# Performance work log

Hardware: AMD Instinct MI355X
Metric: run time of the kernel (lower is better)

## Reference

```python
import jax, jax.numpy as jnp
import numpy as np

B, S, D, E, F, K = 2, 1024, 2048, 8, 1024, 2


def setup_inputs() -> dict:
    key = jax.random.key(0)
    ks = jax.random.split(key, 5)
    s = 0.02  # init scale for weights
    return {
        "hidden_states": jax.random.normal(ks[0], (B, S, D), dtype=jnp.float32),
        "gate_w": jax.random.normal(ks[1], (E, D), dtype=jnp.float32) * s,
        "w_gate": jax.random.normal(ks[2], (E, D, F), dtype=jnp.float32) * s,
        "w_up": jax.random.normal(ks[3], (E, D, F), dtype=jnp.float32) * s,
        "w_down": jax.random.normal(ks[4], (E, F, D), dtype=jnp.float32) * s,
        "top_k": K,
    }


def reference(hidden_states, gate_w, w_gate, w_up, w_down, top_k):
    b, s, d = hidden_states.shape
    x = hidden_states.reshape(-1, d)                      # [T, D] tokens
    T = x.shape[0]
    n_exp = gate_w.shape[0]

    # router gate (bias-free linear) + topk softmax
    router_logits = jnp.einsum('td,ed->te', x, gate_w)    # [T, E]
    probs = jax.nn.softmax(router_logits, axis=-1)
    top_w, top_i = jax.lax.top_k(probs, top_k)            # [T, K]
    top_w = top_w / jnp.sum(top_w, axis=-1, keepdims=True)  # renormalize over selected experts

    # scatter routing weights into dense combine matrix [T, E] (zero for unselected experts)
    comb = jnp.zeros((T, n_exp), dtype=x.dtype)
    comb = comb.at[jnp.arange(T)[:, None], top_i].set(top_w)

    # SwiGLU expert MLPs, computed for all experts and masked by routing weights
    g = jax.nn.silu(jnp.einsum('td,edf->etf', x, w_gate))  # [E, T, F]
    u = jnp.einsum('td,edf->etf', x, w_up)                 # [E, T, F]
    h = (g * u) * comb.T[:, :, None]                       # weight before down-proj to fuse combine
    y = jnp.einsum('etf,efd->td', h, w_down)               # [T, D] combined output

    final = y.reshape(b, s, d)
    return final, router_logits
```

## Files before the change

kernel.cpp:

```cpp
#include <hip/hip_runtime.h>
#include <hip/hip_bf16.h>

#define T_TOK 2048
#define D_DIM 2048
#define N_EXP 8
#define F_DIM 1024

typedef __attribute__((ext_vector_type(8))) short short8;
typedef __attribute__((ext_vector_type(4))) float floatx4;

__device__ __forceinline__ short f2bf(float f) {
  union { float f; unsigned u; } v; v.f = f;
  unsigned r = v.u + 0x7fffu + ((v.u >> 16) & 1u);
  return (short)(r >> 16);
}

__device__ __forceinline__ floatx4 mfma16(short8 a, short8 b, floatx4 c) {
  return __builtin_amdgcn_mfma_f32_16x16x32_bf16(a, b, c, 0, 0, 0);
}

__device__ __forceinline__ void gload16(const void* g, void* l) {
  __builtin_amdgcn_global_load_lds(
      (const __attribute__((address_space(1))) unsigned int*)g,
      (__attribute__((address_space(3))) unsigned int*)l, 16, 0, 0);
}

__global__ __launch_bounds__(256) void transpose_cvt(const float* __restrict__ src,
                                                     short* __restrict__ dst,
                                                     int R, int C) {
  __shared__ float tile[32][33];
  int e = blockIdx.z;
  src += (size_t)e * R * C;
  dst += (size_t)e * R * C;
  int c0 = blockIdx.x * 32, r0 = blockIdx.y * 32;
  int tx = threadIdx.x & 31, ty = threadIdx.x >> 5;
#pragma unroll
  for (int i = 0; i < 32; i += 8)
    tile[ty + i][tx] = src[(size_t)(r0 + ty + i) * C + c0 + tx];
  __syncthreads();
#pragma unroll
  for (int i = 0; i < 32; i += 8)
    dst[(size_t)(c0 + ty + i) * R + r0 + tx] = f2bf(tile[tx][ty + i]);
}

__global__ __launch_bounds__(256) void router_kernel(
    const float* __restrict__ x, const float* __restrict__ gate_w,
    short* __restrict__ x_bf, float* __restrict__ out_logits,
    int* __restrict__ counts, int* __restrict__ tok_ids, float* __restrict__ tok_wts) {
  int t = blockIdx.x;
  int tid = threadIdx.x;
  const float* xr = x + (size_t)t * D_DIM + tid * 8;
  floatx4 xv0 = *(const floatx4*)xr;
  floatx4 xv1 = *(const floatx4*)(xr + 4);
  float xs[8];
#pragma unroll
  for (int j = 0; j < 4; j++) { xs[j] = xv0[j]; xs[4 + j] = xv1[j]; }
  union { short8 v; short s[8]; } xb;
#pragma unroll
  for (int j = 0; j < 8; j++) xb.s[j] = f2bf(xs[j]);
  *(short8*)(x_bf + (size_t)t * D_DIM + tid * 8) = xb.v;

  float p[N_EXP];
#pragma unroll
  for (int e = 0; e < N_EXP; e++) {
    const float* gw = gate_w + (size_t)e * D_DIM + tid * 8;
    floatx4 g0 = *(const floatx4*)gw;
    floatx4 g1 = *(const floatx4*)(gw + 4);
    float s = 0.f;
#pragma unroll
    for (int j = 0; j < 4; j++) s += xs[j] * g0[j] + xs[4 + j] * g1[j];
    p[e] = s;
  }
  __shared__ float red[N_EXP * 4];
  __shared__ float slog[N_EXP];
  int lane = tid & 63, wv = tid >> 6;
#pragma unroll
  for (int e = 0; e < N_EXP; e++) {
    float v = p[e];
#pragma unroll
    for (int off = 32; off > 0; off >>= 1) v += __shfl_down(v, off);
    if (lane == 0) red[e * 4 + wv] = v;
  }
  __syncthreads();
  if (tid < N_EXP) {
    float s = red[tid * 4] + red[tid * 4 + 1] + red[tid * 4 + 2] + red[tid * 4 + 3];
    slog[tid] = s;
    out_logits[(size_t)t * N_EXP + tid] = s;
  }
  __syncthreads();
  if (tid == 0) {
    float l[N_EXP];
#pragma unroll
    for (int e = 0; e < N_EXP; e++) l[e] = slog[e];
    int e0 = 0;
#pragma unroll
    for (int e = 1; e < N_EXP; e++) if (l[e] > l[e0]) e0 = e;
    int e1 = (e0 == 0) ? 1 : 0;
#pragma unroll
    for (int e = 0; e < N_EXP; e++) if (e != e0 && l[e] > l[e1]) e1 = e;
    float p1 = __expf(l[e1] - l[e0]);
    float s = 1.f + p1;
    int pos0 = atomicAdd(&counts[e0], 1);
    tok_ids[e0 * T_TOK + pos0] = t;
    tok_wts[e0 * T_TOK + pos0] = 1.f / s;
    int pos1 = atomicAdd(&counts[e1], 1);
    tok_ids[e1 * T_TOK + pos1] = t | (1 << 16);
    tok_wts[e1 * T_TOK + pos1] = p1 / s;
  }
}

__global__ __launch_bounds__(256, 2) void gemm1_kernel(
    const short* __restrict__ x_bf,
    const short* __restrict__ wgT, const short* __restrict__ wuT,
    const int* __restrict__ counts, const int* __restrict__ tok_ids,
    const float* __restrict__ tok_wts,
    short* __restrict__ hbuf) {
  int e = blockIdx.x >> 4;
  int mt = blockIdx.x & 15;
  int count = counts[e];
  if (mt * 128 >= count) return;
  int f0 = blockIdx.y * 128;

  __shared__ short sA[128 * 64];
  __shared__ short sBg[128 * 64];
  __shared__ short sBu[128 * 64];
  __shared__ int s_tok[128];
  __shared__ float s_wt[128];

  int tid = threadIdx.x;
  if (tid < 128) {
    int r = mt * 128 + tid;
    if (r < count) { s_tok[tid] = tok_ids[e * T_TOK + r]; s_wt[tid] = tok_wts[e * T_TOK + r]; }
    else { s_tok[tid] = 0; s_wt[tid] = 0.f; }
  }
  __syncthreads();

  int lane = tid & 63, wv = tid >> 6;
  int wr = wv >> 1, wc = wv & 1;
  int l16 = lane & 15, qd = lane >> 4;
  int lr = lane >> 3, lc = lane & 7;
  int csw8 = (lc ^ lr) * 8;

  int offA[4], offB[4];
#pragma unroll
  for (int it = 0; it < 4; it++) {
    int r = wv * 32 + it * 8 + lr;
    offA[it] = (s_tok[r] & 0xFFFF) * D_DIM + csw8;
    offB[it] = (e * F_DIM + f0 + r) * D_DIM + csw8;
  }
  short* sdA  = sA  + wv * 2048;
  short* sdBg = sBg + wv * 2048;
  short* sdBu = sBu + wv * 2048;

  floatx4 accG[4][4] = {};
  floatx4 accU[4][4] = {};

  const short* rA  = sA  + (wr * 64 + l16) * 64;
  const short* rBg = sBg + (wc * 64 + l16) * 64;
  const short* rBu = sBu + (wc * 64 + l16) * 64;
  int sw = l16 & 7;

  for (int d0 = 0; d0 < D_DIM; d0 += 64) {
    __syncthreads();
#pragma unroll
    for (int it = 0; it < 4; it++) {
      gload16(x_bf + offA[it] + d0, sdA  + it * 512);
      gload16(wgT  + offB[it] + d0, sdBg + it * 512);
      gload16(wuT  + offB[it] + d0, sdBu + it * 512);
    }
    __syncthreads();
#pragma unroll
    for (int kk = 0; kk < 2; kk++) {
      short8 a[4], bg[4], bu[4];
      int c = ((kk * 4 + qd) ^ sw) * 8;
#pragma unroll
      for (int mi = 0; mi < 4; mi++) a[mi] = *(const short8*)(rA + mi * 16 * 64 + c);
#pragma unroll
      for (int nj = 0; nj < 4; nj++) {
        bg[nj] = *(const short8*)(rBg + nj * 16 * 64 + c);
        bu[nj] = *(const short8*)(rBu + nj * 16 * 64 + c);
      }
#pragma unroll
      for (int mi = 0; mi < 4; mi++)
#pragma unroll
        for (int nj = 0; nj < 4; nj++) {
          accG[mi][nj] = mfma16(a[mi], bg[nj], accG[mi][nj]);
          accU[mi][nj] = mfma16(a[mi], bu[nj], accU[mi][nj]);
        }
    }
  }

#pragma unroll
  for (int mi = 0; mi < 4; mi++)
#pragma unroll
    for (int r = 0; r < 4; r++) {
      int rowl = wr * 64 + mi * 16 + qd * 4 + r;
      if (mt * 128 + rowl < count) {
        int raw = s_tok[rowl];
        int hrow = (raw & 0xFFFF) * 2 + (raw >> 16);
        float wt = s_wt[rowl];
        short* hdst = hbuf + (size_t)hrow * F_DIM + f0 + wc * 64 + l16;
#pragma unroll
        for (int nj = 0; nj < 4; nj++) {
          float g = accG[mi][nj][r], u = accU[mi][nj][r];
          float sg = g / (1.f + __expf(-g));
          hdst[nj * 16] = f2bf(sg * u * wt);
        }
      }
    }
}

__global__ __launch_bounds__(256, 2) void gemm2_kernel(
    const short* __restrict__ hbuf, const short* __restrict__ wdT,
    const int* __restrict__ counts, const int* __restrict__ tok_ids,
    float* __restrict__ outY) {
  int e = blockIdx.x >> 4;
  int mt = blockIdx.x & 15;
  int count = counts[e];
  if (mt * 128 >= count) return;
  int n0 = blockIdx.y * 128;

  __shared__ short sA[128 * 64];
  __shared__ short sB[128 * 64];
  __shared__ int s_tok[128];

  int tid = threadIdx.x;
  if (tid < 128) {
    int r = mt * 128 + tid;
    s_tok[tid] = (r < count) ? tok_ids[e * T_TOK + r] : 0;
  }
  __syncthreads();

  int lane = tid & 63, wv = tid >> 6;
  int wr = wv >> 1, wc = wv & 1;
  int l16 = lane & 15, qd = lane >> 4;
  int lr = lane >> 3, lc = lane & 7;
  int csw8 = (lc ^ lr) * 8;

  int offA[4], offB[4];
#pragma unroll
  for (int it = 0; it < 4; it++) {
    int r = wv * 32 + it * 8 + lr;
    int raw = s_tok[r];
    offA[it] = ((raw & 0xFFFF) * 2 + (raw >> 16)) * F_DIM + csw8;
    offB[it] = (e * D_DIM + n0 + r) * F_DIM + csw8;
  }
  short* sdA = sA + wv * 2048;
  short* sdB = sB + wv * 2048;

  floatx4 acc[4][4] = {};

  const short* rA = sA + (wr * 64 + l16) * 64;
  const short* rB = sB + (wc * 64 + l16) * 64;
  int sw = l16 & 7;

  for (int k0 = 0; k0 < F_DIM; k0 += 64) {
    __syncthreads();
#pragma unroll
    for (int it = 0; it < 4; it++) {
      gload16(hbuf + offA[it] + k0, sdA + it * 512);
      gload16(wdT  + offB[it] + k0, sdB + it * 512);
    }
    __syncthreads();
#pragma unroll
    for (int kk = 0; kk < 2; kk++) {
      short8 a[4], b[4];
      int c = ((kk * 4 + qd) ^ sw) * 8;
#pragma unroll
      for (int mi = 0; mi < 4; mi++) a[mi] = *(const short8*)(rA + mi * 16 * 64 + c);
#pragma unroll
      for (int nj = 0; nj < 4; nj++) b[nj] = *(const short8*)(rB + nj * 16 * 64 + c);
#pragma unroll
      for (int mi = 0; mi < 4; mi++)
#pragma unroll
        for (int nj = 0; nj < 4; nj++)
          acc[mi][nj] = mfma16(a[mi], b[nj], acc[mi][nj]);
    }
  }

#pragma unroll
  for (int mi = 0; mi < 4; mi++)
#pragma unroll
    for (int r = 0; r < 4; r++) {
      int rowl = wr * 64 + mi * 16 + qd * 4 + r;
      if (mt * 128 + rowl < count) {
        int tok = s_tok[rowl] & 0xFFFF;
        float* dst = outY + (size_t)tok * D_DIM + n0 + wc * 64 + l16;
#pragma unroll
        for (int nj = 0; nj < 4; nj++)
          unsafeAtomicAdd(&dst[nj * 16], acc[mi][nj][r]);
      }
    }
}

extern "C" void kernel_launch(void* const* d_in, const int* in_sizes, int n_in,
                              void* d_out, int out_size, void* d_ws, size_t ws_size,
                              hipStream_t stream) {
  (void)in_sizes; (void)n_in; (void)out_size; (void)ws_size;
  const float* hidden = (const float*)d_in[0];
  const float* gate_w = (const float*)d_in[1];
  const float* w_gate = (const float*)d_in[2];
  const float* w_up   = (const float*)d_in[3];
  const float* w_down = (const float*)d_in[4];
  float* out = (float*)d_out;
  float* outY = out;
  float* outLogits = out + (size_t)T_TOK * D_DIM;

  char* ws = (char*)d_ws;
  size_t off = 0;
  int* counts = (int*)(ws + off); off += 256;
  int* tok_ids = (int*)(ws + off); off += (size_t)N_EXP * T_TOK * 4;
  float* tok_wts = (float*)(ws + off); off += (size_t)N_EXP * T_TOK * 4;
  short* x_bf = (short*)(ws + off); off += (size_t)T_TOK * D_DIM * 2;
  short* wgT = (short*)(ws + off); off += (size_t)N_EXP * F_DIM * D_DIM * 2;
  short* wuT = (short*)(ws + off); off += (size_t)N_EXP * F_DIM * D_DIM * 2;
  short* wdT = (short*)(ws + off); off += (size_t)N_EXP * D_DIM * F_DIM * 2;
  short* hbuf = (short*)(ws + off); off += (size_t)T_TOK * 2 * F_DIM * 2;

  hipMemsetAsync(counts, 0, 256, stream);
  hipMemsetAsync(outY, 0, (size_t)T_TOK * D_DIM * 4, stream);

  transpose_cvt<<<dim3(F_DIM / 32, D_DIM / 32, N_EXP), 256, 0, stream>>>(w_gate, wgT, D_DIM, F_DIM);
  transpose_cvt<<<dim3(F_DIM / 32, D_DIM / 32, N_EXP), 256, 0, stream>>>(w_up,   wuT, D_DIM, F_DIM);
  transpose_cvt<<<dim3(D_DIM / 32, F_DIM / 32, N_EXP), 256, 0, stream>>>(w_down, wdT, F_DIM, D_DIM);

  router_kernel<<<T_TOK, 256, 0, stream>>>(hidden, gate_w, x_bf, outLogits,
                                           counts, tok_ids, tok_wts);

  gemm1_kernel<<<dim3(N_EXP * 16, F_DIM / 128), 256, 0, stream>>>(
      x_bf, wgT, wuT, counts, tok_ids, tok_wts, hbuf);

  gemm2_kernel<<<dim3(N_EXP * 16, D_DIM / 128), 256, 0, stream>>>(
      hbuf, wdT, counts, tok_ids, outY);
}
```

Baseline: 497.0 us.

## Multi-buffer LDS tiles to overlap global loads with MFMA in both expert GEMMs

The gate/up GEMM now uses a three-stage LDS ring. It issues loads two K-steps ahead and waits on vmcnt only for the oldest stage, with a single barrier per step. The down-projection GEMM moves to a double-buffered scheme that prefetches the next K-slice before computing the current one, so each step needs one barrier instead of two. The aim is to hide global-to-LDS latency behind matrix-core work. The cost is much more LDS per block, about 144KB in gemm1, which likely allows only one resident block per CU despite the launch bound asking for two.

```diff
diff --git a/kernel.cpp b/kernel.cpp
--- a/kernel.cpp
+++ b/kernel.cpp
@@ -8,6 +8,9 @@
 
 typedef __attribute__((ext_vector_type(8))) short short8;
 typedef __attribute__((ext_vector_type(4))) float floatx4;
+
+#define WAIT_VM12 0xF7C
+#define WAIT_VM0  0xF70
 
 __device__ __forceinline__ short f2bf(float f) {
   union { float f; unsigned u; } v; v.f = f;
@@ -121,9 +124,9 @@
   if (mt * 128 >= count) return;
   int f0 = blockIdx.y * 128;
 
-  __shared__ short sA[128 * 64];
-  __shared__ short sBg[128 * 64];
-  __shared__ short sBu[128 * 64];
+  __shared__ short sA[3][8192];
+  __shared__ short sBg[3][8192];
+  __shared__ short sBu[3][8192];
   __shared__ int s_tok[128];
   __shared__ float s_wt[128];
 
@@ -148,27 +151,24 @@
     offA[it] = (s_tok[r] & 0xFFFF) * D_DIM + csw8;
     offB[it] = (e * F_DIM + f0 + r) * D_DIM + csw8;
   }
-  short* sdA  = sA  + wv * 2048;
-  short* sdBg = sBg + wv * 2048;
-  short* sdBu = sBu + wv * 2048;
 
   floatx4 accG[4][4] = {};
   floatx4 accU[4][4] = {};
-
-  const short* rA  = sA  + (wr * 64 + l16) * 64;
-  const short* rBg = sBg + (wc * 64 + l16) * 64;
-  const short* rBu = sBu + (wc * 64 + l16) * 64;
   int sw = l16 & 7;
 
-  for (int d0 = 0; d0 < D_DIM; d0 += 64) {
-    __syncthreads();
+  auto issueStep = [&](int s, int b) {
+    int d0 = s * 64;
 #pragma unroll
     for (int it = 0; it < 4; it++) {
-      gload16(x_bf + offA[it] + d0, sdA  + it * 512);
-      gload16(wgT  + offB[it] + d0, sdBg + it * 512);
-      gload16(wuT  + offB[it] + d0, sdBu + it * 512);
-    }
-    __syncthreads();
+      gload16(x_bf + offA[it] + d0, &sA[b][wv * 2048 + it * 512]);
+      gload16(wgT  + offB[it] + d0, &sBg[b][wv * 2048 + it * 512]);
+      gload16(wuT  + offB[it] + d0, &sBu[b][wv * 2048 + it * 512]);
+    }
+  };
+  auto computeStep = [&](int b) {
+    const short* rA  = &sA[b][(wr * 64 + l16) * 64];
+    const short* rBg = &sBg[b][(wc * 64 + l16) * 64];
+    const short* rBu = &sBu[b][(wc * 64 + l16) * 64];
 #pragma unroll
     for (int kk = 0; kk < 2; kk++) {
       short8 a[4], bg[4], bu[4];
@@ -188,6 +188,17 @@
           accU[mi][nj] = mfma16(a[mi], bu[nj], accU[mi][nj]);
         }
     }
+  };
+
+  const int NS = D_DIM / 64;
+  issueStep(0, 0);
+  issueStep(1, 1);
+  for (int s = 0; s < NS; s++) {
+    if (s + 1 < NS) __builtin_amdgcn_s_waitcnt(WAIT_VM12);
+    else            __builtin_amdgcn_s_waitcnt(WAIT_VM0);
+    __builtin_amdgcn_s_barrier();
+    if (s + 2 < NS) issueStep(s + 2, (s + 2) % 3);
+    computeStep(s % 3);
   }
 
 #pragma unroll
@@ -220,8 +231,8 @@
   if (mt * 128 >= count) return;
   int n0 = blockIdx.y * 128;
 
-  __shared__ short sA[128 * 64];
-  __shared__ short sB[128 * 64];
+  __shared__ short sA[2][8192];
+  __shared__ short sB[2][8192];
   __shared__ int s_tok[128];
 
   int tid = threadIdx.x;
@@ -245,23 +256,26 @@
     offA[it] = ((raw & 0xFFFF) * 2 + (raw >> 16)) * F_DIM + csw8;
     offB[it] = (e * D_DIM + n0 + r) * F_DIM + csw8;
   }
-  short* sdA = sA + wv * 2048;
-  short* sdB = sB + wv * 2048;
 
   floatx4 acc[4][4] = {};
-
-  const short* rA = sA + (wr * 64 + l16) * 64;
-  const short* rB = sB + (wc * 64 + l16) * 64;
   int sw = l16 & 7;
 
-  for (int k0 = 0; k0 < F_DIM; k0 += 64) {
+  auto issueStep = [&](int s, int b) {
+    int k0 = s * 64;
+#pragma unroll
+    for (int it = 0; it < 4; it++) {
+      gload16(hbuf + offA[it] + k0, &sA[b][wv * 2048 + it * 512]);
+      gload16(wdT  + offB[it] + k0, &sB[b][wv * 2048 + it * 512]);
+    }
+  };
+
+  const int NS = F_DIM / 64;
+  issueStep(0, 0);
+  for (int s = 0; s < NS; s++) {
     __syncthreads();
-#pragma unroll
-    for (int it = 0; it < 4; it++) {
-      gload16(hbuf + offA[it] + k0, sdA + it * 512);
-      gload16(wdT  + offB[it] + k0, sdB + it * 512);
-    }
-    __syncthreads();
+    if (s + 1 < NS) issueStep(s + 1, (s + 1) & 1);
+    const short* rA = &sA[s & 1][(wr * 64 + l16) * 64];
+    const short* rB = &sB[s & 1][(wc * 64 + l16) * 64];
 #pragma unroll
     for (int kk = 0; kk < 2; kk++) {
       short8 a[4], b[4];
```

New measurement: 641.9 us. 1.29x slower.

## Pre-tile expert weights, store sorted expert outputs, replace atomics with combine kernel

Applied to the files above, without the earlier changes.

Weights are repacked into contiguous per-block 64-wide K tiles, so GEMM loads for each B tile read one contiguous chunk. GEMM1 now writes h in expert-sorted row order and uses 64-wide F tiles, which doubles its grid. GEMM2 writes fp32 results to a sorted buffer with plain stores instead of atomics onto the output, which also removes the output memset. A tok2row map and a combine kernel then sum each token's two expert rows. The cost is an extra 32MB fp32 intermediate write and read, two added launches, and a single-block tok2row kernel.

```diff
diff --git a/kernel.cpp b/kernel.cpp
--- a/kernel.cpp
+++ b/kernel.cpp
@@ -25,22 +25,37 @@
       (__attribute__((address_space(3))) unsigned int*)l, 16, 0, 0);
 }
 
-__global__ __launch_bounds__(256) void transpose_cvt(const float* __restrict__ src,
-                                                     short* __restrict__ dst,
-                                                     int R, int C) {
-  __shared__ float tile[32][33];
-  int e = blockIdx.z;
-  src += (size_t)e * R * C;
-  dst += (size_t)e * R * C;
-  int c0 = blockIdx.x * 32, r0 = blockIdx.y * 32;
-  int tx = threadIdx.x & 31, ty = threadIdx.x >> 5;
-#pragma unroll
-  for (int i = 0; i < 32; i += 8)
-    tile[ty + i][tx] = src[(size_t)(r0 + ty + i) * C + c0 + tx];
-  __syncthreads();
-#pragma unroll
-  for (int i = 0; i < 32; i += 8)
-    dst[(size_t)(c0 + ty + i) * R + r0 + tx] = f2bf(tile[tx][ty + i]);
+__global__ __launch_bounds__(256) void pack_wgwu(const float* __restrict__ src,
+                                                 short* __restrict__ dst) {
+  int fb = blockIdx.x, s = blockIdx.y, e = blockIdx.z;
+  __shared__ float tile[64][65];
+  int tx = threadIdx.x & 63, ty = threadIdx.x >> 6;
+  const float* sp = src + (size_t)e * D_DIM * F_DIM + (size_t)(s * 64) * F_DIM + fb * 64;
+#pragma unroll
+  for (int i = 0; i < 64; i += 4)
+    tile[ty + i][tx] = sp[(size_t)(ty + i) * F_DIM + tx];
+  __syncthreads();
+  short* dp = dst + (size_t)((e * 16 + fb) * 32 + s) * 4096;
+#pragma unroll
+  for (int i = 0; i < 64; i += 4)
+    dp[(ty + i) * 64 + tx] = f2bf(tile[tx][ty + i]);
+}
+
+__global__ __launch_bounds__(256) void pack_wd(const float* __restrict__ src,
+                                               short* __restrict__ dst) {
+  int nb = blockIdx.x, s = blockIdx.y, e = blockIdx.z;
+  __shared__ float tile[64][129];
+  int tx2 = threadIdx.x & 127, ty2 = threadIdx.x >> 7;
+  const float* sp = src + (size_t)e * F_DIM * D_DIM + (size_t)(s * 64) * D_DIM + nb * 128;
+#pragma unroll
+  for (int i = 0; i < 64; i += 2)
+    tile[ty2 + i][tx2] = sp[(size_t)(ty2 + i) * D_DIM + tx2];
+  __syncthreads();
+  int tx = threadIdx.x & 63, ty = threadIdx.x >> 6;
+  short* dp = dst + (size_t)((e * 16 + nb) * 16 + s) * 8192;
+#pragma unroll
+  for (int r = 0; r < 128; r += 4)
+    dp[(r + ty) * 64 + tx] = f2bf(tile[tx][r + ty]);
 }
 
 __global__ __launch_bounds__(256) void router_kernel(
@@ -109,21 +124,39 @@
   }
 }
 
+__global__ __launch_bounds__(256) void tok2row_kernel(
+    const int* __restrict__ counts, const int* __restrict__ tok_ids,
+    int* __restrict__ tok2row) {
+  int tid = threadIdx.x;
+  int base = 0;
+  for (int e = 0; e < N_EXP; e++) {
+    int c = counts[e];
+    for (int pos = tid; pos < c; pos += 256) {
+      int raw = tok_ids[e * T_TOK + pos];
+      tok2row[(raw & 0xFFFF) * 2 + (raw >> 16)] = base + pos;
+    }
+    base += c;
+  }
+}
+
 __global__ __launch_bounds__(256, 2) void gemm1_kernel(
     const short* __restrict__ x_bf,
-    const short* __restrict__ wgT, const short* __restrict__ wuT,
+    const short* __restrict__ pwg, const short* __restrict__ pwu,
     const int* __restrict__ counts, const int* __restrict__ tok_ids,
     const float* __restrict__ tok_wts,
-    short* __restrict__ hbuf) {
+    short* __restrict__ h_sorted) {
   int e = blockIdx.x >> 4;
   int mt = blockIdx.x & 15;
   int count = counts[e];
   if (mt * 128 >= count) return;
-  int f0 = blockIdx.y * 128;
-
-  __shared__ short sA[128 * 64];
-  __shared__ short sBg[128 * 64];
-  __shared__ short sBu[128 * 64];
+  int fb = blockIdx.y;
+  int hb = 0;
+#pragma unroll
+  for (int i = 0; i < N_EXP; i++) { int c = counts[i]; if (i < e) hb += c; }
+
+  __shared__ short sA[8192];
+  __shared__ short sBg[4096];
+  __shared__ short sBu[4096];
   __shared__ int s_tok[128];
   __shared__ float s_wt[128];
 
@@ -141,49 +174,51 @@
   int lr = lane >> 3, lc = lane & 7;
   int csw8 = (lc ^ lr) * 8;
 
-  int offA[4], offB[4];
+  int offA[4], offB[2];
 #pragma unroll
   for (int it = 0; it < 4; it++) {
     int r = wv * 32 + it * 8 + lr;
     offA[it] = (s_tok[r] & 0xFFFF) * D_DIM + csw8;
-    offB[it] = (e * F_DIM + f0 + r) * D_DIM + csw8;
-  }
-  short* sdA  = sA  + wv * 2048;
-  short* sdBg = sBg + wv * 2048;
-  short* sdBu = sBu + wv * 2048;
-
-  floatx4 accG[4][4] = {};
-  floatx4 accU[4][4] = {};
-
+  }
+#pragma unroll
+  for (int it = 0; it < 2; it++)
+    offB[it] = (wv * 16 + it * 8 + lr) * 64 + csw8;
+  const short* pBg = pwg + (size_t)((e * 16 + fb) * 32) * 4096;
+  const short* pBu = pwu + (size_t)((e * 16 + fb) * 32) * 4096;
+
+  floatx4 accG[4][2] = {};
+  floatx4 accU[4][2] = {};
+  int sw = l16 & 7;
   const short* rA  = sA  + (wr * 64 + l16) * 64;
-  const short* rBg = sBg + (wc * 64 + l16) * 64;
-  const short* rBu = sBu + (wc * 64 + l16) * 64;
-  int sw = l16 & 7;
-
-  for (int d0 = 0; d0 < D_DIM; d0 += 64) {
+  const short* rBg = sBg + (wc * 32 + l16) * 64;
+  const short* rBu = sBu + (wc * 32 + l16) * 64;
+
+  for (int s = 0; s < D_DIM / 64; s++) {
     __syncthreads();
 #pragma unroll
-    for (int it = 0; it < 4; it++) {
-      gload16(x_bf + offA[it] + d0, sdA  + it * 512);
-      gload16(wgT  + offB[it] + d0, sdBg + it * 512);
-      gload16(wuT  + offB[it] + d0, sdBu + it * 512);
+    for (int it = 0; it < 4; it++)
+      gload16(x_bf + offA[it] + s * 64, sA + wv * 2048 + it * 512);
+#pragma unroll
+    for (int it = 0; it < 2; it++) {
+      gload16(pBg + (size_t)s * 4096 + offB[it], sBg + wv * 1024 + it * 512);
+      gload16(pBu + (size_t)s * 4096 + offB[it], sBu + wv * 1024 + it * 512);
     }
     __syncthreads();
 #pragma unroll
     for (int kk = 0; kk < 2; kk++) {
-      short8 a[4], bg[4], bu[4];
+      short8 a[4], bg[2], bu[2];
       int c = ((kk * 4 + qd) ^ sw) * 8;
 #pragma unroll
       for (int mi = 0; mi < 4; mi++) a[mi] = *(const short8*)(rA + mi * 16 * 64 + c);
 #pragma unroll
-      for (int nj = 0; nj < 4; nj++) {
+      for (int nj = 0; nj < 2; nj++) {
         bg[nj] = *(const short8*)(rBg + nj * 16 * 64 + c);
         bu[nj] = *(const short8*)(rBu + nj * 16 * 64 + c);
       }
 #pragma unroll
       for (int mi = 0; mi < 4; mi++)
 #pragma unroll
-        for (int nj = 0; nj < 4; nj++) {
+        for (int nj = 0; nj < 2; nj++) {
           accG[mi][nj] = mfma16(a[mi], bg[nj], accG[mi][nj]);
           accU[mi][nj] = mfma16(a[mi], bu[nj], accU[mi][nj]);
         }
@@ -196,12 +231,11 @@
     for (int r = 0; r < 4; r++) {
       int rowl = wr * 64 + mi * 16 + qd * 4 + r;
       if (mt * 128 + rowl < count) {
-        int raw = s_tok[rowl];
-        int hrow = (raw & 0xFFFF) * 2 + (raw >> 16);
         float wt = s_wt[rowl];
-        short* hdst = hbuf + (size_t)hrow * F_DIM + f0 + wc * 64 + l16;
-#pragma unroll
-        for (int nj = 0; nj < 4; nj++) {
+        short* hdst = h_sorted + (size_t)(hb + mt * 128 + rowl) * F_DIM
+                    + fb * 64 + wc * 32 + l16;
+#pragma unroll
+        for (int nj = 0; nj < 2; nj++) {
           float g = accG[mi][nj][r], u = accU[mi][nj][r];
           float sg = g / (1.f + __expf(-g));
           hdst[nj * 16] = f2bf(sg * u * wt);
@@ -211,26 +245,22 @@
 }
 
 __global__ __launch_bounds__(256, 2) void gemm2_kernel(
-    const short* __restrict__ hbuf, const short* __restrict__ wdT,
-    const int* __restrict__ counts, const int* __restrict__ tok_ids,
-    float* __restrict__ outY) {
+    const short* __restrict__ h_sorted, const short* __restrict__ pwd,
+    const int* __restrict__ counts,
+    float* __restrict__ y_sorted) {
   int e = blockIdx.x >> 4;
   int mt = blockIdx.x & 15;
   int count = counts[e];
   if (mt * 128 >= count) return;
-  int n0 = blockIdx.y * 128;
-
-  __shared__ short sA[128 * 64];
-  __shared__ short sB[128 * 64];
-  __shared__ int s_tok[128];
+  int nb = blockIdx.y;
+  int hb = 0;
+#pragma unroll
+  for (int i = 0; i < N_EXP; i++) { int c = counts[i]; if (i < e) hb += c; }
+
+  __shared__ short sA[8192];
+  __shared__ short sB[8192];
 
   int tid = threadIdx.x;
-  if (tid < 128) {
-    int r = mt * 128 + tid;
-    s_tok[tid] = (r < count) ? tok_ids[e * T_TOK + r] : 0;
-  }
-  __syncthreads();
-
   int lane = tid & 63, wv = tid >> 6;
   int wr = wv >> 1, wc = wv & 1;
   int l16 = lane & 15, qd = lane >> 4;
@@ -241,25 +271,22 @@
 #pragma unroll
   for (int it = 0; it < 4; it++) {
     int r = wv * 32 + it * 8 + lr;
-    int raw = s_tok[r];
-    offA[it] = ((raw & 0xFFFF) * 2 + (raw >> 16)) * F_DIM + csw8;
-    offB[it] = (e * D_DIM + n0 + r) * F_DIM + csw8;
-  }
-  short* sdA = sA + wv * 2048;
-  short* sdB = sB + wv * 2048;
+    offA[it] = (hb + mt * 128 + r) * F_DIM + csw8;
+    offB[it] = r * 64 + csw8;
+  }
+  const short* pB = pwd + (size_t)((e * 16 + nb) * 16) * 8192;
 
   floatx4 acc[4][4] = {};
-
+  int sw = l16 & 7;
   const short* rA = sA + (wr * 64 + l16) * 64;
   const short* rB = sB + (wc * 64 + l16) * 64;
-  int sw = l16 & 7;
-
-  for (int k0 = 0; k0 < F_DIM; k0 += 64) {
+
+  for (int s = 0; s < F_DIM / 64; s++) {
     __syncthreads();
 #pragma unroll
     for (int it = 0; it < 4; it++) {
-      gload16(hbuf + offA[it] + k0, sdA + it * 512);
-      gload16(wdT  + offB[it] + k0, sdB + it * 512);
+      gload16(h_sorted + offA[it] + s * 64, sA + wv * 2048 + it * 512);
+      gload16(pB + (size_t)s * 8192 + offB[it], sB + wv * 2048 + it * 512);
     }
     __syncthreads();
 #pragma unroll
@@ -284,13 +311,26 @@
     for (int r = 0; r < 4; r++) {
       int rowl = wr * 64 + mi * 16 + qd * 4 + r;
       if (mt * 128 + rowl < count) {
-        int tok = s_tok[rowl] & 0xFFFF;
-        float* dst = outY + (size_t)tok * D_DIM + n0 + wc * 64 + l16;
+        float* dst = y_sorted + (size_t)(hb + mt * 128 + rowl) * D_DIM
+                   + nb * 128 + wc * 64 + l16;
 #pragma unroll
         for (int nj = 0; nj < 4; nj++)
-          unsafeAtomicAdd(&dst[nj * 16], acc[mi][nj][r]);
+          dst[nj * 16] = acc[mi][nj][r];
       }
     }
+}
+
+__global__ __launch_bounds__(256) void combine_kernel(
+    const float* __restrict__ y_sorted, const int* __restrict__ tok2row,
+    float* __restrict__ outY) {
+  int t = blockIdx.x;
+  int r0 = tok2row[t * 2], r1 = tok2row[t * 2 + 1];
+  int i = threadIdx.x * 8;
+  const floatx4* a = (const floatx4*)(y_sorted + (size_t)r0 * D_DIM + i);
+  const floatx4* b = (const floatx4*)(y_sorted + (size_t)r1 * D_DIM + i);
+  floatx4* o = (floatx4*)(outY + (size_t)t * D_DIM + i);
+  o[0] = a[0] + b[0];
+  o[1] = a[1] + b[1];
 }
 
 extern "C" void kernel_launch(void* const* d_in, const int* in_sizes, int n_in,
@@ -311,25 +351,29 @@
   int* counts = (int*)(ws + off); off += 256;
   int* tok_ids = (int*)(ws + off); off += (size_t)N_EXP * T_TOK * 4;
   float* tok_wts = (float*)(ws + off); off += (size_t)N_EXP * T_TOK * 4;
+  int* tok2row = (int*)(ws + off); off += (size_t)T_TOK * 2 * 4;
   short* x_bf = (short*)(ws + off); off += (size_t)T_TOK * D_DIM * 2;
-  short* wgT = (short*)(ws + off); off += (size_t)N_EXP * F_DIM * D_DIM * 2;
-  short* wuT = (short*)(ws + off); off += (size_t)N_EXP * F_DIM * D_DIM * 2;
-  short* wdT = (short*)(ws + off); off += (size_t)N_EXP * D_DIM * F_DIM * 2;
-  short* hbuf = (short*)(ws + off); off += (size_t)T_TOK * 2 * F_DIM * 2;
+  short* pwg = (short*)(ws + off); off += (size_t)N_EXP * F_DIM * D_DIM * 2;
+  short* pwu = (short*)(ws + off); off += (size_t)N_EXP * F_DIM * D_DIM * 2;
+  short* pwd = (short*)(ws + off); off += (size_t)N_EXP * D_DIM * F_DIM * 2;
+  short* h_sorted = (short*)(ws + off); off += (size_t)T_TOK * 2 * F_DIM * 2;
+  float* y_sorted = (float*)(ws + off); off += (size_t)T_TOK * 2 * D_DIM * 4;
 
   hipMemsetAsync(counts, 0, 256, stream);
-  hipMemsetAsync(outY, 0, (size_t)T_TOK * D_DIM * 4, stream);
-
-  transpose_cvt<<<dim3(F_DIM / 32, D_DIM / 32, N_EXP), 256, 0, stream>>>(w_gate, wgT, D_DIM, F_DIM);
-  transpose_cvt<<<dim3(F_DIM / 32, D_DIM / 32, N_EXP), 256, 0, stream>>>(w_up,   wuT, D_DIM, F_DIM);
-  transpose_cvt<<<dim3(D_DIM / 32, F_DIM / 32, N_EXP), 256, 0, stream>>>(w_down, wdT, F_DIM, D_DIM);
+
+  pack_wgwu<<<dim3(16, 32, N_EXP), 256, 0, stream>>>(w_gate, pwg);
+  pack_wgwu<<<dim3(16, 32, N_EXP), 256, 0, stream>>>(w_up, pwu);
+  pack_wd<<<dim3(16, 16, N_EXP), 256, 0, stream>>>(w_down, pwd);
 
   router_kernel<<<T_TOK, 256, 0, stream>>>(hidden, gate_w, x_bf, outLogits,
                                            counts, tok_ids, tok_wts);
-
-  gemm1_kernel<<<dim3(N_EXP * 16, F_DIM / 128), 256, 0, stream>>>(
-      x_bf, wgT, wuT, counts, tok_ids, tok_wts, hbuf);
+  tok2row_kernel<<<1, 256, 0, stream>>>(counts, tok_ids, tok2row);
+
+  gemm1_kernel<<<dim3(N_EXP * 16, F_DIM / 64), 256, 0, stream>>>(
+      x_bf, pwg, pwu, counts, tok_ids, tok_wts, h_sorted);
 
   gemm2_kernel<<<dim3(N_EXP * 16, D_DIM / 128), 256, 0, stream>>>(
-      hbuf, wdT, counts, tok_ids, outY);
-}
+      h_sorted, pwd, counts, y_sorted);
+
+  combine_kernel<<<T_TOK, 256, 0, stream>>>(y_sorted, tok2row, outY);
+}
```

New measurement: 480.4 us. 3.3% less time.
